# Kernel tuning notes

Measured on AMD Instinct MI355X. Metric: run time of the kernel, lower is better.

## Reference

```python
import jax, jax.numpy as jnp
import numpy as np

B, S, D, H = 32, 2048, 128, 16  # batch, cached kv len, head dim (=d_model), heads
EPS = 1e-5


def setup_inputs() -> dict:
    key = jax.random.key(0)
    ks = jax.random.split(key, 5)
    d_total = D * H
    x = jax.random.normal(ks[0], (B, 1, D), jnp.float32)
    past_k = jax.random.normal(ks[1], (B, H, S, D), jnp.float32)
    past_v = jax.random.normal(ks[2], (B, H, S, D), jnp.float32)
    Wqkv = jax.random.normal(ks[3], (3 * d_total, D), jnp.float32) * 0.02
    bqkv = jnp.zeros((3 * d_total,), jnp.float32)
    Wout = jax.random.normal(ks[4], (D, d_total), jnp.float32) * 0.02
    bout = jnp.zeros((D,), jnp.float32)
    return {"x": x, "past_k": past_k, "past_v": past_v,
            "Wqkv": Wqkv, "bqkv": bqkv, "Wout": Wout, "bout": bout}


def reference(x, past_k, past_v, Wqkv, bqkv, Wout, bout):
    # QKV projection: (B,1,D) -> (B,1,3*H*D)
    qkv = x @ Wqkv.T + bqkv
    qkv = qkv.reshape(B, 1, 3 * H, D).transpose(0, 2, 1, 3)  # (B,3H,1,D)
    q, k_new, v_new = jnp.split(qkv, 3, axis=1)              # each (B,H,1,D)
    k = jnp.concatenate([past_k, k_new], axis=2)             # (B,H,S+1,D)
    v = jnp.concatenate([past_v, v_new], axis=2)
    # single-query attention (causal mask is trivially all-visible for q_len=1)
    scale = 1.0 / jnp.sqrt(jnp.float32(D))
    scores = jnp.einsum('bhqd,bhkd->bhqk', q, k) * scale     # (B,H,1,S+1)
    probs = jax.nn.softmax(scores, axis=-1)
    y = jnp.einsum('bhqk,bhkd->bhqd', probs, v)              # (B,H,1,D)
    y = y.transpose(0, 2, 1, 3).reshape(B, 1, H * D)         # (B,1,H*D)
    y = y @ Wout.T + bout                                    # (B,1,D)
    y = y + x                                                # residual
    # layer norm over last dim, no affine params
    mu = jnp.mean(y, axis=-1, keepdims=True)
    var = jnp.mean(jnp.square(y - mu), axis=-1, keepdims=True)
    out = (y - mu) / jnp.sqrt(var + EPS)
    return (out, k, v)
```

## Files before the change

### kernel.cpp

```cpp
#include <hip/hip_runtime.h>
#include <math.h>

#define B 32
#define S 2048
#define S1 2049
#define D 128
#define H 16
#define DT 2048
#define EPS 1e-5f
#define SCALE 0.08838834764831845f

typedef float f4v __attribute__((ext_vector_type(4)));

__global__ void __launch_bounds__(256)
qkv_proj_kernel(const float* __restrict__ x,
                const float* __restrict__ Wqkv,
                const float* __restrict__ bqkv,
                float* __restrict__ qkv,
                float* __restrict__ out_k,
                float* __restrict__ out_v) {
    const int b = blockIdx.x;
    const int j = blockIdx.y * 256 + threadIdx.x;
    __shared__ float xs[D];
    if (threadIdx.x < D) xs[threadIdx.x] = x[b * D + threadIdx.x];
    __syncthreads();
    const float* w = Wqkv + (size_t)j * D;
    float acc = bqkv[j];
#pragma unroll
    for (int d = 0; d < D; d += 4) {
        float4 w4 = *reinterpret_cast<const float4*>(w + d);
        acc = fmaf(w4.x, xs[d + 0], acc);
        acc = fmaf(w4.y, xs[d + 1], acc);
        acc = fmaf(w4.z, xs[d + 2], acc);
        acc = fmaf(w4.w, xs[d + 3], acc);
    }
    qkv[(size_t)b * (3 * DT) + j] = acc;

    if (j >= DT) {
        const int r = j - DT;
        const int which = r >> 11;
        const int hd = r & (DT - 1);
        const int h = hd >> 7;
        const int d = hd & 127;
        float* dst = which ? out_v : out_k;
        dst[((size_t)(b * H + h) * S1 + S) * D + d] = acc;
    }
}

__global__ void __launch_bounds__(1024)
attn_kernel(const float* __restrict__ past_k,
            const float* __restrict__ past_v,
            const float* __restrict__ qkv,
            float* __restrict__ out_k,
            float* __restrict__ out_v,
            float* __restrict__ ys_g) {
    const int bh = blockIdx.x;
    const int b = bh >> 4;
    const int h = bh & (H - 1);
    const int tid  = threadIdx.x;
    const int wave = tid >> 6;
    const int lane = tid & 63;
    const int l32  = tid & 31;
    const int rg   = tid >> 5;

    __shared__ float sc[S1 + 3];
    __shared__ float swm[16];
    __shared__ float swl[16];
    __shared__ float sacc[32 * D];

    const f4v* __restrict__ kin  = (const f4v*)past_k + (size_t)bh * S * 32;
    const f4v* __restrict__ vin  = (const f4v*)past_v + (size_t)bh * S * 32;
    f4v* __restrict__ kout = (f4v*)out_k + (size_t)bh * S1 * 32;
    f4v* __restrict__ vout = (f4v*)out_v + (size_t)bh * S1 * 32;

    const float* qp   = qkv + (size_t)b * (3 * DT) + h * D;
    const float* knew = qp + DT;
    const float* vnew = qp + 2 * DT;

    const f4v q4 = ((const f4v*)qp)[l32];

#pragma unroll 8
    for (int it = 0; it < S / 32; ++it) {
        const int r = it * 32 + rg;
        const size_t off = (size_t)r * 32 + l32;
        f4v k4 = __builtin_nontemporal_load(&kin[off]);
        __builtin_nontemporal_store(k4, &kout[off]);
        f4v t = k4 * q4;
        float p = t.x + t.y + t.z + t.w;
        p += __shfl_xor(p, 1);
        p += __shfl_xor(p, 2);
        p += __shfl_xor(p, 4);
        p += __shfl_xor(p, 8);
        p += __shfl_xor(p, 16);
        if (l32 == 0) sc[r] = p * SCALE;
    }
    if (tid < 64) {
        float pd = qp[2 * tid] * knew[2 * tid] + qp[2 * tid + 1] * knew[2 * tid + 1];
        pd += __shfl_xor(pd, 1);
        pd += __shfl_xor(pd, 2);
        pd += __shfl_xor(pd, 4);
        pd += __shfl_xor(pd, 8);
        pd += __shfl_xor(pd, 16);
        pd += __shfl_xor(pd, 32);
        if (tid == 0) sc[S] = pd * SCALE;
    }
    __syncthreads();

    const float s0v = sc[tid];
    const float s1v = sc[tid + 1024];
    const float sxv = (tid == 0) ? sc[S] : -1e30f;
    float m = fmaxf(fmaxf(s0v, s1v), sxv);
#pragma unroll
    for (int off = 1; off < 64; off <<= 1) m = fmaxf(m, __shfl_xor(m, off));
    if (lane == 0) swm[wave] = m;
    __syncthreads();
    float M = swm[0];
#pragma unroll
    for (int g = 1; g < 16; ++g) M = fmaxf(M, swm[g]);
    const float e0 = __expf(s0v - M);
    const float e1 = __expf(s1v - M);
    sc[tid] = e0;
    sc[tid + 1024] = e1;
    float lsum = e0 + e1;
    if (tid == 0) {
        const float e2 = __expf(sxv - M);
        sc[S] = e2;
        lsum += e2;
    }
#pragma unroll
    for (int off = 1; off < 64; off <<= 1) lsum += __shfl_xor(lsum, off);
    if (lane == 0) swl[wave] = lsum;
    __syncthreads();
    float L = swl[0];
#pragma unroll
    for (int g = 1; g < 16; ++g) L += swl[g];
    const float invL = 1.0f / L;

    f4v acc = (f4v){0.f, 0.f, 0.f, 0.f};
#pragma unroll 8
    for (int it = 0; it < S / 32; ++it) {
        const int r = it * 32 + rg;
        const size_t off = (size_t)r * 32 + l32;
        f4v v4 = __builtin_nontemporal_load(&vin[off]);
        __builtin_nontemporal_store(v4, &vout[off]);
        acc += v4 * sc[r];
    }

    ((f4v*)sacc)[rg * 32 + l32] = acc;
    __syncthreads();

    if (tid < D) {
        float y = 0.f;
#pragma unroll
        for (int g = 0; g < 32; ++g) y += sacc[g * D + tid];
        y = fmaf(sc[S], vnew[tid], y);
        ys_g[(size_t)bh * D + tid] = y * invL;
    }
}

__global__ void __launch_bounds__(1024)
out_proj_kernel(const float* __restrict__ x,
                const float* __restrict__ ys_g,
                const float* __restrict__ Wout,
                const float* __restrict__ bout,
                float* __restrict__ out) {
    const int b = blockIdx.x;
    const int t = threadIdx.x;
    __shared__ float ys[DT];
    __shared__ float pp[D * 8];
    __shared__ float tb[D];

    ys[t]        = ys_g[(size_t)b * DT + t];
    ys[t + 1024] = ys_g[(size_t)b * DT + t + 1024];
    __syncthreads();

    {
        const int d = t >> 3;
        const int sub = t & 7;
        const float* w = Wout + (size_t)d * DT + sub * 256;
        const float* y = ys + sub * 256;
        float acc = 0.f;
#pragma unroll
        for (int j = 0; j < 256; j += 4) {
            float4 w4 = *reinterpret_cast<const float4*>(w + j);
            acc = fmaf(w4.x, y[j + 0], acc);
            acc = fmaf(w4.y, y[j + 1], acc);
            acc = fmaf(w4.z, y[j + 2], acc);
            acc = fmaf(w4.w, y[j + 3], acc);
        }
        pp[d * 8 + sub] = acc;
    }
    __syncthreads();

    float val = 0.f;
    if (t < D) {
        float a = 0.f;
#pragma unroll
        for (int g = 0; g < 8; ++g) a += pp[t * 8 + g];
        val = a + bout[t] + x[b * D + t];
        tb[t] = val;
    }
    __syncthreads();
    for (int off = 64; off > 0; off >>= 1) {
        if (t < off) tb[t] += tb[t + off];
        __syncthreads();
    }
    const float mu = tb[0] * (1.0f / D);
    __syncthreads();
    const float diff = val - mu;
    if (t < D) tb[t] = diff * diff;
    __syncthreads();
    for (int off = 64; off > 0; off >>= 1) {
        if (t < off) tb[t] += tb[t + off];
        __syncthreads();
    }
    const float var = tb[0] * (1.0f / D);
    if (t < D) out[(size_t)b * D + t] = diff / sqrtf(var + EPS);
}

extern "C" void kernel_launch(void* const* d_in, const int* in_sizes, int n_in,
                              void* d_out, int out_size, void* d_ws, size_t ws_size,
                              hipStream_t stream) {
    const float* x      = (const float*)d_in[0];
    const float* past_k = (const float*)d_in[1];
    const float* past_v = (const float*)d_in[2];
    const float* Wqkv   = (const float*)d_in[3];
    const float* bqkv   = (const float*)d_in[4];
    const float* Wout   = (const float*)d_in[5];
    const float* bout   = (const float*)d_in[6];

    float* out   = (float*)d_out;
    float* out_k = out + (size_t)B * D;
    float* out_v = out_k + (size_t)B * H * S1 * D;

    float* qkv  = (float*)d_ws;
    float* ys_g = qkv + (size_t)B * 3 * DT;

    qkv_proj_kernel<<<dim3(B, (3 * DT) / 256), 256, 0, stream>>>(
        x, Wqkv, bqkv, qkv, out_k, out_v);
    attn_kernel<<<B * H, 1024, 0, stream>>>(
        past_k, past_v, qkv, out_k, out_v, ys_g);
    out_proj_kernel<<<B, 1024, 0, stream>>>(
        x, ys_g, Wout, bout, out);
}
```

Baseline: 445.3 us.

## Fuse QKV projection into attention kernel and use regular stores for KV copy

Drops the separate QKV projection kernel. Each attention block now computes its own head's q, k_new and v_new (384 rows of Wqkv) into shared memory, saving one launch and the global round-trip of the qkv buffer. It also switches the K/V cache copy stores from nontemporal to regular stores. The cost is a serial matvec prologue in every block before streaming starts, and Wqkv rows are re-read by all 32 batch blocks of each head.

```diff
diff --git a/kernel.cpp b/kernel.cpp
--- a/kernel.cpp
+++ b/kernel.cpp
@@ -12,45 +12,12 @@
 
 typedef float f4v __attribute__((ext_vector_type(4)));
 
-__global__ void __launch_bounds__(256)
-qkv_proj_kernel(const float* __restrict__ x,
-                const float* __restrict__ Wqkv,
-                const float* __restrict__ bqkv,
-                float* __restrict__ qkv,
-                float* __restrict__ out_k,
-                float* __restrict__ out_v) {
-    const int b = blockIdx.x;
-    const int j = blockIdx.y * 256 + threadIdx.x;
-    __shared__ float xs[D];
-    if (threadIdx.x < D) xs[threadIdx.x] = x[b * D + threadIdx.x];
-    __syncthreads();
-    const float* w = Wqkv + (size_t)j * D;
-    float acc = bqkv[j];
-#pragma unroll
-    for (int d = 0; d < D; d += 4) {
-        float4 w4 = *reinterpret_cast<const float4*>(w + d);
-        acc = fmaf(w4.x, xs[d + 0], acc);
-        acc = fmaf(w4.y, xs[d + 1], acc);
-        acc = fmaf(w4.z, xs[d + 2], acc);
-        acc = fmaf(w4.w, xs[d + 3], acc);
-    }
-    qkv[(size_t)b * (3 * DT) + j] = acc;
-
-    if (j >= DT) {
-        const int r = j - DT;
-        const int which = r >> 11;
-        const int hd = r & (DT - 1);
-        const int h = hd >> 7;
-        const int d = hd & 127;
-        float* dst = which ? out_v : out_k;
-        dst[((size_t)(b * H + h) * S1 + S) * D + d] = acc;
-    }
-}
-
 __global__ void __launch_bounds__(1024)
-attn_kernel(const float* __restrict__ past_k,
+attn_kernel(const float* __restrict__ x,
+            const float* __restrict__ Wqkv,
+            const float* __restrict__ bqkv,
+            const float* __restrict__ past_k,
             const float* __restrict__ past_v,
-            const float* __restrict__ qkv,
             float* __restrict__ out_k,
             float* __restrict__ out_v,
             float* __restrict__ ys_g) {
@@ -63,6 +30,8 @@
     const int l32  = tid & 31;
     const int rg   = tid >> 5;
 
+    __shared__ float xs[D];
+    __shared__ float qkvs[3 * D];
     __shared__ float sc[S1 + 3];
     __shared__ float swm[16];
     __shared__ float swl[16];
@@ -73,18 +42,36 @@
     f4v* __restrict__ kout = (f4v*)out_k + (size_t)bh * S1 * 32;
     f4v* __restrict__ vout = (f4v*)out_v + (size_t)bh * S1 * 32;
 
-    const float* qp   = qkv + (size_t)b * (3 * DT) + h * D;
-    const float* knew = qp + DT;
-    const float* vnew = qp + 2 * DT;
-
-    const f4v q4 = ((const f4v*)qp)[l32];
+    if (tid < D) xs[tid] = x[b * D + tid];
+    __syncthreads();
+    if (tid < 3 * D) {
+        const int which = tid >> 7;
+        const int d = tid & 127;
+        const int row = which * DT + h * D + d;
+        const float* w = Wqkv + (size_t)row * D;
+        float acc = bqkv[row];
+#pragma unroll
+        for (int j = 0; j < D; j += 4) {
+            float4 w4 = *reinterpret_cast<const float4*>(w + j);
+            acc = fmaf(w4.x, xs[j + 0], acc);
+            acc = fmaf(w4.y, xs[j + 1], acc);
+            acc = fmaf(w4.z, xs[j + 2], acc);
+            acc = fmaf(w4.w, xs[j + 3], acc);
+        }
+        qkvs[tid] = acc;
+        if (which == 1) ((float*)kout)[(size_t)S * D + d] = acc;
+        if (which == 2) ((float*)vout)[(size_t)S * D + d] = acc;
+    }
+    __syncthreads();
+
+    const f4v q4 = ((const f4v*)qkvs)[l32];
 
 #pragma unroll 8
     for (int it = 0; it < S / 32; ++it) {
         const int r = it * 32 + rg;
         const size_t off = (size_t)r * 32 + l32;
         f4v k4 = __builtin_nontemporal_load(&kin[off]);
-        __builtin_nontemporal_store(k4, &kout[off]);
+        kout[off] = k4;
         f4v t = k4 * q4;
         float p = t.x + t.y + t.z + t.w;
         p += __shfl_xor(p, 1);
@@ -95,7 +82,8 @@
         if (l32 == 0) sc[r] = p * SCALE;
     }
     if (tid < 64) {
-        float pd = qp[2 * tid] * knew[2 * tid] + qp[2 * tid + 1] * knew[2 * tid + 1];
+        float pd = qkvs[2 * tid] * qkvs[D + 2 * tid]
+                 + qkvs[2 * tid + 1] * qkvs[D + 2 * tid + 1];
         pd += __shfl_xor(pd, 1);
         pd += __shfl_xor(pd, 2);
         pd += __shfl_xor(pd, 4);
@@ -142,7 +130,7 @@
         const int r = it * 32 + rg;
         const size_t off = (size_t)r * 32 + l32;
         f4v v4 = __builtin_nontemporal_load(&vin[off]);
-        __builtin_nontemporal_store(v4, &vout[off]);
+        vout[off] = v4;
         acc += v4 * sc[r];
     }
 
@@ -153,7 +141,7 @@
         float y = 0.f;
 #pragma unroll
         for (int g = 0; g < 32; ++g) y += sacc[g * D + tid];
-        y = fmaf(sc[S], vnew[tid], y);
+        y = fmaf(sc[S], qkvs[2 * D + tid], y);
         ys_g[(size_t)bh * D + tid] = y * invL;
     }
 }
@@ -233,13 +221,10 @@
     float* out_k = out + (size_t)B * D;
     float* out_v = out_k + (size_t)B * H * S1 * D;
 
-    float* qkv  = (float*)d_ws;
-    float* ys_g = qkv + (size_t)B * 3 * DT;
-
-    qkv_proj_kernel<<<dim3(B, (3 * DT) / 256), 256, 0, stream>>>(
-        x, Wqkv, bqkv, qkv, out_k, out_v);
+    float* ys_g = (float*)d_ws;
+
     attn_kernel<<<B * H, 1024, 0, stream>>>(
-        past_k, past_v, qkv, out_k, out_v, ys_g);
+        x, Wqkv, bqkv, past_k, past_v, out_k, out_v, ys_g);
     out_proj_kernel<<<B, 1024, 0, stream>>>(
         x, ys_g, Wout, bout, out);
 }
```

After: 441.3 us (median of 2 runs). About the same (-0.9%).
